# Kernel tuning notes

Measured on AMD Instinct MI355X. Metric: run time of the kernel, lower is better.

Reference implementation:

```python
import jax, jax.numpy as jnp
import numpy as np

B, L, A, K = 2, 1024, 14, 30
NUM_RBF = 16
NPE = 16  # num_positional_embeddings
EF = 128  # edge_features
EDGE_IN = NPE + NUM_RBF * A * A  # 3152


def setup_inputs() -> dict:
    key = jax.random.key(0)
    ks = jax.random.split(key, 4)
    # coords scaled so pairwise distances span the RBF range [0, 20]
    X = jax.random.normal(ks[0], (B, L, A, 3), dtype=jnp.float32) * 3.0
    mask = jnp.ones((B, L), dtype=jnp.float32)
    residue_idx = jnp.tile(jnp.arange(L, dtype=jnp.int32)[None, :], (B, 1))
    chain_labels = jnp.zeros((B, L), dtype=jnp.int32)
    atom_mask = jax.random.randint(ks[1], (B, L, A), 0, 2).astype(jnp.float32)
    W_edge = jax.random.normal(ks[2], (EF, EDGE_IN), dtype=jnp.float32) * 0.02
    ln_gamma = jnp.ones((EF,), dtype=jnp.float32)
    ln_beta = jnp.zeros((EF,), dtype=jnp.float32)
    return {"X": X, "mask": mask, "residue_idx": residue_idx,
            "chain_labels": chain_labels, "atom_mask": atom_mask,
            "W_edge": W_edge, "ln_gamma": ln_gamma, "ln_beta": ln_beta}


def reference(X, mask, residue_idx, chain_labels, atom_mask, W_edge, ln_gamma, ln_beta):
    Bq, Lq = X.shape[0], X.shape[1]
    # ---- CA pairwise distances + masked top-k (smallest) ----
    X_ca = X[:, :, 1, :]
    m2 = mask[:, :, None] * mask[:, None, :]                    # [B,L,L]
    dX = X_ca[:, :, None, :] - X_ca[:, None, :, :]
    D = m2 * jnp.sqrt(jnp.sum(dX ** 2, -1) + 1e-6)
    D_max = jnp.max(D, -1, keepdims=True)
    D_adjust = D + 2.0 * (1.0 - m2) * D_max
    _, E_idx = jax.lax.top_k(-D_adjust, K)                      # smallest K -> [B,L,K]
    # ---- transformer positional encoding of relative index ----
    ii = jnp.arange(Lq, dtype=jnp.float32)[None, :, None]
    d = (E_idx.astype(jnp.float32) - ii)[..., None]             # [B,L,K,1]
    freq = jnp.exp(jnp.arange(0, NPE, 2, dtype=jnp.float32) * (-(np.log(10000.0) / NPE)))
    angles = d * freq                                           # [B,L,K,NPE/2]
    E_pos = jnp.concatenate([jnp.cos(angles), jnp.sin(angles)], -1)  # [B,L,K,NPE]
    # ---- impute CB, build 14-atom set ----
    N_, Ca, C_, O_ = X[:, :, 0, :], X[:, :, 1, :], X[:, :, 2, :], X[:, :, 3, :]
    b = Ca - N_
    c = C_ - Ca
    a = jnp.cross(b, c)
    Cb = -0.58273431 * a + 0.56802827 * b - 0.54067466 * c + Ca
    X2 = jnp.concatenate([jnp.stack([N_, Ca, C_, O_, Cb], -2), X[:, :, 5:, :]], -2)  # [B,L,14,3]
    am = 1.0 - atom_mask                                        # module passes 1 - atom_mask
    # ---- gather neighbor atoms, fused 14x14 atom-pair RBFs ----
    bidx = jnp.arange(Bq)[:, None, None]
    X2n = X2[bidx, E_idx]                                       # [B,L,K,14,3]
    amn = am[bidx, E_idx]                                       # [B,L,K,14]
    diff = X2[:, :, None, :, None, :] - X2n[:, :, :, None, :, :]
    Dab = jnp.sqrt(jnp.sum(diff ** 2, -1) + 1e-6)               # [B,L,K,14,14] (a of i, b of nbr)
    combo = am[:, :, None, :, None] * amn[:, :, :, None, :]     # [B,L,K,14,14]
    mu = jnp.linspace(0.0, 20.0, NUM_RBF)
    sigma = 20.0 / NUM_RBF
    rbf = jnp.exp(-(((Dab[..., None] - mu) / sigma) ** 2)) * combo[..., None]
    RBF_all = rbf.reshape(Bq, Lq, K, A * A * NUM_RBF)           # matches torch cat order (i,j,rbf)
    # ---- edge embedding + layernorm ----
    E = jnp.concatenate([E_pos, RBF_all], -1)                   # [B,L,K,EDGE_IN]
    E = E @ W_edge.T                                            # [B,L,K,EF]
    mean = jnp.mean(E, -1, keepdims=True)
    var = jnp.var(E, -1, keepdims=True)
    E = (E - mean) / jnp.sqrt(var + 1e-5) * ln_gamma + ln_beta
    return (E, E_idx)
```

## Files before the change

kernel.cpp:

```cpp
#include <hip/hip_runtime.h>
#include <hip/hip_bf16.h>
#include <stdint.h>

#define LQ 1024
#define BQ 2
#define AQ 14
#define KQ 30
#define EFQ 128
#define EDGE_IN 3152
#define KPAD 3200
#define NCHUNK 50
#define ROWS (BQ*LQ*KQ)
#define EIDX_OFF (ROWS*EFQ)

typedef __attribute__((ext_vector_type(8))) short short8;
typedef __attribute__((ext_vector_type(4))) float floatx4;
using bf16_t = __hip_bfloat16;
typedef unsigned long long ull;

static __device__ __forceinline__ unsigned short f2bf(float f) {
    __hip_bfloat16 h = __float2bfloat16(f);
    return *reinterpret_cast<unsigned short*>(&h);
}

__global__ __launch_bounds__(256) void topk_kernel(
    const float* __restrict__ X, const float* __restrict__ mask,
    float* __restrict__ out, int* __restrict__ idx_ws)
{
    const int lane = threadIdx.x & 63;
    const int row  = blockIdx.x*4 + (threadIdx.x >> 6);
    const int b = row >> 10, i = row & (LQ - 1);

    size_t cb = ((size_t)(b*LQ + i))*42 + 3;
    const float cxf = X[cb], cyf = X[cb+1], czf = X[cb+2];
    const float mif = mask[b*LQ + i];
    const double cx = (double)cxf, cy = (double)cyf, cz = (double)czf;

    double Dk[16];
    float  mf[16];
    bool allone = (mif == 1.0f);
    #pragma unroll
    for (int s = 0; s < 16; ++s) {
        int j = s*64 + lane;
        size_t base = ((size_t)(b*LQ + j))*42 + 3;
        float xj = X[base+0], yj = X[base+1], zj = X[base+2];
        mf[s] = mask[b*LQ + j];
        double dx = __dsub_rn(cx, (double)xj);
        double dy = __dsub_rn(cy, (double)yj);
        double dz = __dsub_rn(cz, (double)zj);
        Dk[s] = __dadd_rn(__dadd_rn(__dmul_rn(dx,dx), __dmul_rn(dy,dy)),
                          __dmul_rn(dz,dz));
        allone = allone && (mf[s] == 1.0f);
    }

    if (!__all(allone ? 1 : 0)) {
        const double mi_d = (double)mif;
        double lmax = 0.0;
        #pragma unroll
        for (int s = 0; s < 16; ++s) {
            double m2 = __dmul_rn(mi_d, (double)mf[s]);
            Dk[s] = __dmul_rn(m2, sqrt(__dadd_rn(Dk[s], 1e-6)));
            lmax = fmax(lmax, Dk[s]);
        }
        #pragma unroll
        for (int off = 32; off; off >>= 1) lmax = fmax(lmax, __shfl_xor(lmax, off));
        #pragma unroll
        for (int s = 0; s < 16; ++s) {
            double m2 = __dmul_rn(mi_d, (double)mf[s]);
            Dk[s] = __dadd_rn(Dk[s],
                    __dmul_rn(__dmul_rn(2.0, __dsub_rn(1.0, m2)), lmax));
        }
    }

    unsigned cons = 0;
    for (int k = 0; k < KQ; ++k) {
        ull bk = ~0ull; int bi = 1 << 30;
        #pragma unroll
        for (int s = 0; s < 16; ++s) {
            ull key = (ull)__double_as_longlong(Dk[s]);
            bool alive = !((cons >> s) & 1u);
            if (alive && key < bk) { bk = key; bi = s*64 + lane; }
        }
        #pragma unroll
        for (int off = 32; off; off >>= 1) {
            ull okk = __shfl_xor(bk, off);
            int oii = __shfl_xor(bi, off);
            if (okk < bk || (okk == bk && oii < bi)) { bk = okk; bi = oii; }
        }
        if ((bi & 63) == lane) cons |= (1u << (bi >> 6));
        if (lane == 0) {
            int rg = row*KQ + k;
            idx_ws[rg] = bi;
            out[EIDX_OFF + rg] = (float)bi;
        }
    }
}

__global__ __launch_bounds__(256) void wpad_kernel(
    const float* __restrict__ W, bf16_t* __restrict__ wpad)
{
    int idx = blockIdx.x*256 + threadIdx.x;
    if (idx >= EFQ*KPAD) return;
    int n = idx / KPAD, f = idx - n*KPAD;
    float v = (f < EDGE_IN) ? W[(size_t)n*EDGE_IN + f] : 0.0f;
    wpad[idx] = __float2bfloat16(v);
}

struct FusedSmem {
    alignas(16) float atoms[128*42];
    alignas(16) unsigned short Bl[128*64];
    alignas(16) float drow[64];
    int residg[128];
    unsigned int maskb[128];
    float gsh[EFQ], bsh[EFQ];
};

static __device__ __forceinline__ void gen8(
    const FusedSmem& sm, int m, int f0, unsigned short* __restrict__ v)
{
    if (f0 >= 16) {
        int p = (f0 - 16) >> 4;
        if (p >= AQ*AQ) {
            #pragma unroll
            for (int j = 0; j < 8; ++j) v[j] = 0;
            return;
        }
        int rbase = (f0 - 16) & 15;
        int a  = (p * 74899) >> 20;
        int bp = p - a*14;
        float combof = ((((sm.maskb[m] >> a) & 1u) |
                         ((sm.maskb[64+m] >> bp) & 1u)) == 0u) ? 1.0f : 0.0f;
        const float* ca = &sm.atoms[m*42 + a*3];
        const float* na = &sm.atoms[(64+m)*42 + bp*3];
        float dx = ca[0]-na[0], dy = ca[1]-na[1], dz = ca[2]-na[2];
        float dab = sqrtf(dx*dx + dy*dy + dz*dz + 1e-6f);
        float u = dab * 0.96089846f;
        #pragma unroll
        for (int j = 0; j < 8; ++j) {
            float tt = __fmaf_rn(-(float)(rbase + j), 1.28119795f, u);
            float e  = __builtin_amdgcn_exp2f(-(tt*tt));
            v[j] = f2bf(e * combof);
        }
    } else {
        float d = sm.drow[m];
        const float fr[8] = {1.0f, 0.31622776601683794f, 0.1f,
            0.031622776601683794f, 0.01f, 0.0031622776601683794f,
            0.001f, 0.00031622776601683794f};
        if (f0 == 0) {
            #pragma unroll
            for (int j = 0; j < 8; ++j) v[j] = f2bf(__cosf(d * fr[j]));
        } else {
            #pragma unroll
            for (int j = 0; j < 8; ++j) v[j] = f2bf(__sinf(d * fr[j]));
        }
    }
}

__global__ __launch_bounds__(256) void fused_kernel(
    const float* __restrict__ X, const float* __restrict__ atom_mask,
    const bf16_t* __restrict__ wpad, const float* __restrict__ gamma,
    const float* __restrict__ beta, const int* __restrict__ idx_ws,
    float* __restrict__ out)
{
    __shared__ FusedSmem sm;
    const int t = threadIdx.x;
    const int row0 = blockIdx.x * 64;
    const int b = row0 / (LQ*KQ);

    if (t < 64) {
        int rg = row0 + t;
        int rem = rg - b*(LQ*KQ);
        int i = rem / KQ;
        int j = idx_ws[rg];
        sm.residg[t]    = b*LQ + i;
        sm.residg[64+t] = b*LQ + j;
        sm.drow[t] = (float)j - (float)i;
    }
    if (t < EFQ) { sm.gsh[t] = gamma[t]; sm.bsh[t] = beta[t]; }
    __syncthreads();

    for (int u = t; u < 128*42; u += 256) {
        int s = u / 42; int e = u - s*42;
        sm.atoms[s*42 + e] = X[(size_t)sm.residg[s]*42 + e];
    }
    __syncthreads();

    if (t < 128) {
        float* at = &sm.atoms[t*42];
        float Nx=at[0],Ny=at[1],Nz=at[2], Cax=at[3],Cay=at[4],Caz=at[5],
              Cx=at[6],Cy=at[7],Cz=at[8];
        float bx=Cax-Nx, by=Cay-Ny, bz=Caz-Nz;
        float ex=Cx-Cax, ey=Cy-Cay, ez=Cz-Caz;
        float ax = by*ez - bz*ey, ay = bz*ex - bx*ez, az = bx*ey - by*ex;
        at[12] = -0.58273431f*ax + 0.56802827f*bx - 0.54067466f*ex + Cax;
        at[13] = -0.58273431f*ay + 0.56802827f*by - 0.54067466f*ey + Cay;
        at[14] = -0.58273431f*az + 0.56802827f*bz - 0.54067466f*ez + Caz;
        unsigned mb = 0;
        const float* amp = &atom_mask[(size_t)sm.residg[t]*AQ];
        #pragma unroll
        for (int a = 0; a < AQ; ++a) if (amp[a] > 0.5f) mb |= (1u << a);
        sm.maskb[t] = mb;
    }

    const int w = t >> 6, lane = t & 63, q = lane >> 4, l15 = lane & 15;
    const int m = w*16 + l15;

    auto stage = [&](int c) {
        #pragma unroll
        for (int i2 = 0; i2 < 4; ++i2) {
            int region = w*4 + i2;
            int n = region*8 + (lane >> 3);
            int kbsrc = (lane & 7) ^ (lane >> 3);
            const bf16_t* g = wpad + (size_t)n*KPAD + c*64 + kbsrc*8;
            __builtin_amdgcn_global_load_lds(
                (const __attribute__((address_space(1))) uint32_t*)g,
                (__attribute__((address_space(3))) uint32_t*)&sm.Bl[region*512],
                16, 0, 0);
        }
    };

    floatx4 acc[8];
    #pragma unroll
    for (int nt = 0; nt < 8; ++nt) acc[nt] = (floatx4){0.f,0.f,0.f,0.f};

    __syncthreads();

    for (int c = 0; c < NCHUNK; ++c) {
        if (c) __syncthreads();
        stage(c);
        __attribute__((aligned(16))) unsigned short va[16];
        gen8(sm, m, c*64 + q*8,      &va[0]);
        gen8(sm, m, c*64 + 32 + q*8, &va[8]);
        __syncthreads();
        short8 a0 = *reinterpret_cast<short8*>(&va[0]);
        short8 a1 = *reinterpret_cast<short8*>(&va[8]);
        #pragma unroll
        for (int nt = 0; nt < 8; ++nt) {
            int n = nt*16 + l15;
            short8 b0 = *reinterpret_cast<const short8*>(
                &sm.Bl[n*64 + ((q ^ (n&7))*8)]);
            short8 b1 = *reinterpret_cast<const short8*>(
                &sm.Bl[n*64 + (((4+q) ^ (n&7))*8)]);
            acc[nt] = __builtin_amdgcn_mfma_f32_16x16x32_bf16(a0, b0, acc[nt], 0, 0, 0);
            acc[nt] = __builtin_amdgcn_mfma_f32_16x16x32_bf16(a1, b1, acc[nt], 0, 0, 0);
        }
    }

    #pragma unroll
    for (int v = 0; v < 4; ++v) {
        float s = 0.f, s2 = 0.f;
        #pragma unroll
        for (int nt = 0; nt < 8; ++nt) { float x = acc[nt][v]; s += x; s2 += x*x; }
        #pragma unroll
        for (int off = 1; off < 16; off <<= 1) {
            s  += __shfl_xor(s,  off);
            s2 += __shfl_xor(s2, off);
        }
        float mean = s * (1.0f/128.0f);
        float var  = s2 * (1.0f/128.0f) - mean*mean;
        float rstd = 1.0f / sqrtf(var + 1e-5f);
        int row_l = w*16 + q*4 + v;
        size_t obase = (size_t)(row0 + row_l)*EFQ;
        #pragma unroll
        for (int nt = 0; nt < 8; ++nt) {
            int col = nt*16 + l15;
            out[obase + col] = (acc[nt][v] - mean)*rstd*sm.gsh[col] + sm.bsh[col];
        }
    }
}

extern "C" void kernel_launch(void* const* d_in, const int* in_sizes, int n_in,
                              void* d_out, int out_size, void* d_ws, size_t ws_size,
                              hipStream_t stream)
{
    const float* X         = (const float*)d_in[0];
    const float* mask      = (const float*)d_in[1];
    const float* atom_mask = (const float*)d_in[4];
    const float* W         = (const float*)d_in[5];
    const float* gamma     = (const float*)d_in[6];
    const float* beta      = (const float*)d_in[7];
    float* out = (float*)d_out;

    int*    idx_ws = (int*)d_ws;
    bf16_t* wpad   = (bf16_t*)((char*)d_ws + 262144);

    hipLaunchKernelGGL(wpad_kernel, dim3((EFQ*KPAD + 255)/256), dim3(256), 0, stream,
                       W, wpad);
    hipLaunchKernelGGL(topk_kernel, dim3(BQ*LQ/4), dim3(256), 0, stream,
                       X, mask, out, idx_ws);
    hipLaunchKernelGGL(fused_kernel, dim3(ROWS/64), dim3(256), 0, stream,
                       X, atom_mask, wpad, gamma, beta, idx_ws, out);
}
```

Baseline: 204.5 us.

## Split top-k across four waves with merge, switch GEMM operands to fp16

The top-k kernel now assigns one row per 256-thread block. Each of the four waves selects a local top-30 over its quarter of the candidates, and one thread merges the four sorted lists, which raises parallelism and cuts the serial per-wave work. The edge-feature GEMM now uses fp16 operands with packed round-toward-zero conversion (cvt_pkrtz) instead of per-element bf16 conversion, which reduces the conversion instruction count in the feature-generation loop. Switching to fp16 changes rounding behaviour, and the single-thread merge adds a serial tail.

```diff
diff --git a/kernel.cpp b/kernel.cpp
--- a/kernel.cpp
+++ b/kernel.cpp
@@ -13,62 +13,70 @@
 #define ROWS (BQ*LQ*KQ)
 #define EIDX_OFF (ROWS*EFQ)
 
-typedef __attribute__((ext_vector_type(8))) short short8;
+typedef __attribute__((ext_vector_type(8))) _Float16 half8;
 typedef __attribute__((ext_vector_type(4))) float floatx4;
-using bf16_t = __hip_bfloat16;
 typedef unsigned long long ull;
 
-static __device__ __forceinline__ unsigned short f2bf(float f) {
-    __hip_bfloat16 h = __float2bfloat16(f);
-    return *reinterpret_cast<unsigned short*>(&h);
+static __device__ __forceinline__ uint32_t pkh(float a, float b) {
+    auto h = __builtin_amdgcn_cvt_pkrtz(a, b);
+    return __builtin_bit_cast(uint32_t, h);
 }
 
 __global__ __launch_bounds__(256) void topk_kernel(
     const float* __restrict__ X, const float* __restrict__ mask,
     float* __restrict__ out, int* __restrict__ idx_ws)
 {
-    const int lane = threadIdx.x & 63;
-    const int row  = blockIdx.x*4 + (threadIdx.x >> 6);
+    __shared__ ull    klist[4][KQ];
+    __shared__ int    ilist[4][KQ];
+    __shared__ int    aflag[4];
+    __shared__ double lmax_sh[4];
+
+    const int t = threadIdx.x, w = t >> 6, lane = t & 63;
+    const int row = blockIdx.x;
     const int b = row >> 10, i = row & (LQ - 1);
 
     size_t cb = ((size_t)(b*LQ + i))*42 + 3;
-    const float cxf = X[cb], cyf = X[cb+1], czf = X[cb+2];
     const float mif = mask[b*LQ + i];
-    const double cx = (double)cxf, cy = (double)cyf, cz = (double)czf;
-
-    double Dk[16];
-    float  mf[16];
+    const double cx = (double)X[cb], cy = (double)X[cb+1], cz = (double)X[cb+2];
+
+    double Dk[4]; float mf[4];
     bool allone = (mif == 1.0f);
     #pragma unroll
-    for (int s = 0; s < 16; ++s) {
-        int j = s*64 + lane;
+    for (int s = 0; s < 4; ++s) {
+        int j = w*256 + s*64 + lane;
         size_t base = ((size_t)(b*LQ + j))*42 + 3;
-        float xj = X[base+0], yj = X[base+1], zj = X[base+2];
+        double dx = __dsub_rn(cx, (double)X[base+0]);
+        double dy = __dsub_rn(cy, (double)X[base+1]);
+        double dz = __dsub_rn(cz, (double)X[base+2]);
         mf[s] = mask[b*LQ + j];
-        double dx = __dsub_rn(cx, (double)xj);
-        double dy = __dsub_rn(cy, (double)yj);
-        double dz = __dsub_rn(cz, (double)zj);
         Dk[s] = __dadd_rn(__dadd_rn(__dmul_rn(dx,dx), __dmul_rn(dy,dy)),
                           __dmul_rn(dz,dz));
         allone = allone && (mf[s] == 1.0f);
     }
-
-    if (!__all(allone ? 1 : 0)) {
+    int aw = __all(allone ? 1 : 0);
+    if (lane == 0) aflag[w] = aw;
+    __syncthreads();
+    const bool fast = aflag[0] && aflag[1] && aflag[2] && aflag[3];
+
+    if (!fast) {
         const double mi_d = (double)mif;
-        double lmax = 0.0;
-        #pragma unroll
-        for (int s = 0; s < 16; ++s) {
+        double lm = 0.0;
+        #pragma unroll
+        for (int s = 0; s < 4; ++s) {
             double m2 = __dmul_rn(mi_d, (double)mf[s]);
             Dk[s] = __dmul_rn(m2, sqrt(__dadd_rn(Dk[s], 1e-6)));
-            lmax = fmax(lmax, Dk[s]);
-        }
-        #pragma unroll
-        for (int off = 32; off; off >>= 1) lmax = fmax(lmax, __shfl_xor(lmax, off));
-        #pragma unroll
-        for (int s = 0; s < 16; ++s) {
+            lm = fmax(lm, Dk[s]);
+        }
+        #pragma unroll
+        for (int off = 32; off; off >>= 1) lm = fmax(lm, __shfl_xor(lm, off));
+        if (lane == 0) lmax_sh[w] = lm;
+        __syncthreads();
+        double gl = fmax(fmax(lmax_sh[0], lmax_sh[1]), fmax(lmax_sh[2], lmax_sh[3]));
+        #pragma unroll
+        for (int s = 0; s < 4; ++s) {
             double m2 = __dmul_rn(mi_d, (double)mf[s]);
             Dk[s] = __dadd_rn(Dk[s],
-                    __dmul_rn(__dmul_rn(2.0, __dsub_rn(1.0, m2)), lmax));
+                    __dmul_rn(__dmul_rn(2.0, __dsub_rn(1.0, m2)), gl));
         }
     }
 
@@ -76,10 +84,10 @@
     for (int k = 0; k < KQ; ++k) {
         ull bk = ~0ull; int bi = 1 << 30;
         #pragma unroll
-        for (int s = 0; s < 16; ++s) {
+        for (int s = 0; s < 4; ++s) {
             ull key = (ull)__double_as_longlong(Dk[s]);
             bool alive = !((cons >> s) & 1u);
-            if (alive && key < bk) { bk = key; bi = s*64 + lane; }
+            if (alive && key < bk) { bk = key; bi = w*256 + s*64 + lane; }
         }
         #pragma unroll
         for (int off = 32; off; off >>= 1) {
@@ -87,23 +95,38 @@
             int oii = __shfl_xor(bi, off);
             if (okk < bk || (okk == bk && oii < bi)) { bk = okk; bi = oii; }
         }
-        if ((bi & 63) == lane) cons |= (1u << (bi >> 6));
-        if (lane == 0) {
+        if ((bi & 63) == lane) cons |= (1u << ((bi >> 6) & 3));
+        if (lane == 0) { klist[w][k] = bk; ilist[w][k] = bi; }
+    }
+    __syncthreads();
+
+    if (t == 0) {
+        int ptr[4] = {0,0,0,0};
+        ull hk[4]; int hi_[4];
+        #pragma unroll
+        for (int l = 0; l < 4; ++l) { hk[l] = klist[l][0]; hi_[l] = ilist[l][0]; }
+        for (int k = 0; k < KQ; ++k) {
+            int bsel = 0;
+            #pragma unroll
+            for (int l = 1; l < 4; ++l)
+                if (hk[l] < hk[bsel] || (hk[l] == hk[bsel] && hi_[l] < hi_[bsel])) bsel = l;
             int rg = row*KQ + k;
-            idx_ws[rg] = bi;
-            out[EIDX_OFF + rg] = (float)bi;
+            idx_ws[rg] = hi_[bsel];
+            out[EIDX_OFF + rg] = (float)hi_[bsel];
+            if (++ptr[bsel] < KQ) { hk[bsel] = klist[bsel][ptr[bsel]]; hi_[bsel] = ilist[bsel][ptr[bsel]]; }
+            else hk[bsel] = ~0ull;
         }
     }
 }
 
 __global__ __launch_bounds__(256) void wpad_kernel(
-    const float* __restrict__ W, bf16_t* __restrict__ wpad)
+    const float* __restrict__ W, _Float16* __restrict__ wpad)
 {
     int idx = blockIdx.x*256 + threadIdx.x;
     if (idx >= EFQ*KPAD) return;
     int n = idx / KPAD, f = idx - n*KPAD;
     float v = (f < EDGE_IN) ? W[(size_t)n*EDGE_IN + f] : 0.0f;
-    wpad[idx] = __float2bfloat16(v);
+    wpad[idx] = (_Float16)v;
 }
 
 struct FusedSmem {
@@ -116,49 +139,48 @@
 };
 
 static __device__ __forceinline__ void gen8(
-    const FusedSmem& sm, int m, int f0, unsigned short* __restrict__ v)
+    const FusedSmem& sm, int m, int f0, uint32_t* __restrict__ v)
 {
     if (f0 >= 16) {
         int p = (f0 - 16) >> 4;
-        if (p >= AQ*AQ) {
-            #pragma unroll
-            for (int j = 0; j < 8; ++j) v[j] = 0;
-            return;
-        }
+        if (p >= AQ*AQ) { v[0] = v[1] = v[2] = v[3] = 0u; return; }
         int rbase = (f0 - 16) & 15;
         int a  = (p * 74899) >> 20;
         int bp = p - a*14;
-        float combof = ((((sm.maskb[m] >> a) & 1u) |
-                         ((sm.maskb[64+m] >> bp) & 1u)) == 0u) ? 1.0f : 0.0f;
+        bool czero = ((((sm.maskb[m] >> a) | (sm.maskb[64+m] >> bp)) & 1u) != 0u);
         const float* ca = &sm.atoms[m*42 + a*3];
         const float* na = &sm.atoms[(64+m)*42 + bp*3];
         float dx = ca[0]-na[0], dy = ca[1]-na[1], dz = ca[2]-na[2];
-        float dab = sqrtf(dx*dx + dy*dy + dz*dz + 1e-6f);
-        float u = dab * 0.96089846f;
+        float u = __builtin_amdgcn_sqrtf(dx*dx + dy*dy + dz*dz + 1e-6f) * 0.96089846f;
+        float e[8];
         #pragma unroll
         for (int j = 0; j < 8; ++j) {
             float tt = __fmaf_rn(-(float)(rbase + j), 1.28119795f, u);
-            float e  = __builtin_amdgcn_exp2f(-(tt*tt));
-            v[j] = f2bf(e * combof);
-        }
+            e[j] = __builtin_amdgcn_exp2f(-(tt*tt));
+        }
+        #pragma unroll
+        for (int k = 0; k < 4; ++k) v[k] = czero ? 0u : pkh(e[2*k], e[2*k+1]);
     } else {
         float d = sm.drow[m];
         const float fr[8] = {1.0f, 0.31622776601683794f, 0.1f,
             0.031622776601683794f, 0.01f, 0.0031622776601683794f,
             0.001f, 0.00031622776601683794f};
+        float e[8];
         if (f0 == 0) {
             #pragma unroll
-            for (int j = 0; j < 8; ++j) v[j] = f2bf(__cosf(d * fr[j]));
+            for (int j = 0; j < 8; ++j) e[j] = __cosf(d * fr[j]);
         } else {
             #pragma unroll
-            for (int j = 0; j < 8; ++j) v[j] = f2bf(__sinf(d * fr[j]));
-        }
+            for (int j = 0; j < 8; ++j) e[j] = __sinf(d * fr[j]);
+        }
+        #pragma unroll
+        for (int k = 0; k < 4; ++k) v[k] = pkh(e[2*k], e[2*k+1]);
     }
 }
 
 __global__ __launch_bounds__(256) void fused_kernel(
     const float* __restrict__ X, const float* __restrict__ atom_mask,
-    const bf16_t* __restrict__ wpad, const float* __restrict__ gamma,
+    const _Float16* __restrict__ wpad, const float* __restrict__ gamma,
     const float* __restrict__ beta, const int* __restrict__ idx_ws,
     float* __restrict__ out)
 {
@@ -211,7 +233,7 @@
             int region = w*4 + i2;
             int n = region*8 + (lane >> 3);
             int kbsrc = (lane & 7) ^ (lane >> 3);
-            const bf16_t* g = wpad + (size_t)n*KPAD + c*64 + kbsrc*8;
+            const _Float16* g = wpad + (size_t)n*KPAD + c*64 + kbsrc*8;
             __builtin_amdgcn_global_load_lds(
                 (const __attribute__((address_space(1))) uint32_t*)g,
                 (__attribute__((address_space(3))) uint32_t*)&sm.Bl[region*512],
@@ -225,24 +247,23 @@
 
     __syncthreads();
 
+    union H8 { uint32_t u[4]; half8 h; };
     for (int c = 0; c < NCHUNK; ++c) {
         if (c) __syncthreads();
         stage(c);
-        __attribute__((aligned(16))) unsigned short va[16];
-        gen8(sm, m, c*64 + q*8,      &va[0]);
-        gen8(sm, m, c*64 + 32 + q*8, &va[8]);
+        H8 va0, va1;
+        gen8(sm, m, c*64 + q*8,      va0.u);
+        gen8(sm, m, c*64 + 32 + q*8, va1.u);
         __syncthreads();
-        short8 a0 = *reinterpret_cast<short8*>(&va[0]);
-        short8 a1 = *reinterpret_cast<short8*>(&va[8]);
         #pragma unroll
         for (int nt = 0; nt < 8; ++nt) {
             int n = nt*16 + l15;
-            short8 b0 = *reinterpret_cast<const short8*>(
+            half8 b0 = *reinterpret_cast<const half8*>(
                 &sm.Bl[n*64 + ((q ^ (n&7))*8)]);
-            short8 b1 = *reinterpret_cast<const short8*>(
+            half8 b1 = *reinterpret_cast<const half8*>(
                 &sm.Bl[n*64 + (((4+q) ^ (n&7))*8)]);
-            acc[nt] = __builtin_amdgcn_mfma_f32_16x16x32_bf16(a0, b0, acc[nt], 0, 0, 0);
-            acc[nt] = __builtin_amdgcn_mfma_f32_16x16x32_bf16(a1, b1, acc[nt], 0, 0, 0);
+            acc[nt] = __builtin_amdgcn_mfma_f32_16x16x32_f16(va0.h, b0, acc[nt], 0, 0, 0);
+            acc[nt] = __builtin_amdgcn_mfma_f32_16x16x32_f16(va1.h, b1, acc[nt], 0, 0, 0);
         }
     }
 
@@ -281,12 +302,12 @@
     const float* beta      = (const float*)d_in[7];
     float* out = (float*)d_out;
 
-    int*    idx_ws = (int*)d_ws;
-    bf16_t* wpad   = (bf16_t*)((char*)d_ws + 262144);
+    int*       idx_ws = (int*)d_ws;
+    _Float16*  wpad   = (_Float16*)((char*)d_ws + 262144);
 
     hipLaunchKernelGGL(wpad_kernel, dim3((EFQ*KPAD + 255)/256), dim3(256), 0, stream,
                        W, wpad);
-    hipLaunchKernelGGL(topk_kernel, dim3(BQ*LQ/4), dim3(256), 0, stream,
+    hipLaunchKernelGGL(topk_kernel, dim3(BQ*LQ), dim3(256), 0, stream,
                        X, mask, out, idx_ws);
     hipLaunchKernelGGL(fused_kernel, dim3(ROWS/64), dim3(256), 0, stream,
                        X, atom_mask, wpad, gamma, beta, idx_ws, out);
```

Result: slower. 226.4 us (+10.7%).
